# Kernel optimization log

Measured on AMD Instinct MI355X. Metric: run time of the kernel, lower is better.

Reference implementation:

```python
import jax, jax.numpy as jnp
import numpy as np

RADIUS = 8
EPSILON = 0.01


def _diff_x(x, r):
    left = x[..., r:2 * r + 1, :]
    middle = x[..., 2 * r + 1:, :] - x[..., :-2 * r - 1, :]
    right = x[..., -1:, :] - x[..., -2 * r - 1:-r - 1, :]
    return jnp.concatenate([left, middle, right], axis=-2)


def _diff_y(x, r):
    left = x[..., r:2 * r + 1]
    middle = x[..., 2 * r + 1:] - x[..., :-2 * r - 1]
    right = x[..., -1:] - x[..., -2 * r - 1:-r - 1]
    return jnp.concatenate([left, middle, right], axis=-1)


def box_filter(x, r):
    # x: (N, C, H, W) -> windowed mean over (2r+1)x(2r+1) with reflect padding
    x = jnp.pad(x, ((0, 0), (0, 0), (r, r), (r, r)), mode='reflect')
    x = jnp.cumsum(x, axis=-2)
    x = _diff_x(x, r)
    x = jnp.cumsum(x, axis=-1)
    x = _diff_y(x, r)
    return x[..., r:-r, r:-r] / float((2 * r + 1) ** 2)


def setup_inputs() -> dict:
    key = jax.random.key(0)
    k1, k2 = jax.random.split(key)
    B, C, H, W = 4, 3, 1024, 1024
    I = jax.random.uniform(k1, (B, C, H, W), dtype=jnp.float32)
    p = jax.random.uniform(k2, (B, 1, H, W), dtype=jnp.float32)
    return {"I": I, "p": p}


def reference(I, p) -> jnp.ndarray:
    r, eps = RADIUS, EPSILON
    B, C, H, W = I.shape

    mean_I = box_filter(I, r)                     # (B,C,H,W)
    mean_p = box_filter(p, r)                     # (B,1,H,W)
    mean_Ip = box_filter(I * p, r)                # (B,C,H,W)
    cov_Ip = mean_Ip - mean_I * mean_p            # (B,C,H,W)

    # second moments: (B,C,C,H,W) via reshape to (B*C, C, H, W) for the box filter
    II = I[:, :, None] * I[:, None]               # (B,C,C,H,W)
    mean_II = box_filter(II.reshape(B * C, C, H, W), r).reshape(B, C, C, H, W)
    cov_II = mean_II - mean_I[:, :, None] * mean_I[:, None]

    eye = jnp.eye(C, dtype=I.dtype).reshape(1, C, C, 1, 1)
    S = cov_II + eps * eye                        # (B,C,C,H,W)

    # per-pixel CxC solve: move pixel dims to batch
    S_px = jnp.transpose(S, (0, 3, 4, 1, 2))      # (B,H,W,C,C)
    rhs = jnp.transpose(cov_Ip, (0, 2, 3, 1))[..., None]  # (B,H,W,C,1)
    a = jnp.linalg.solve(S_px, rhs)[..., 0]       # (B,H,W,C)
    a = jnp.transpose(a, (0, 3, 1, 2))            # (B,C,H,W)

    a_mean_I = jnp.einsum('bchw,bchw->bhw', a, mean_I)
    b = mean_p - a_mean_I[:, None]                # (B,1,H,W)

    mean_a = box_filter(a, r)
    mean_b = box_filter(b, r)

    q = jnp.einsum('bchw,bchw->bhw', mean_a, I) + mean_b[:, 0]
    return q[:, None]                             # (B,1,H,W)
```

## Files before the change

kernel.cpp:

```cpp
#include <hip/hip_runtime.h>

#define HH 1024
#define WW 1024
#define NB 4
#define RR 8
#define NCH1 13
#define NCH2 4
#define VSEG 8
#define NSEG (HH / VSEG)
#define NBLK (NB * NSEG)
#define NXCD 8
#define CPX (NBLK / NXCD)
#define LDSW 1040
#define INV_AREA (1.0f/289.0f)
#define EPS_REG 0.01f

typedef float f4 __attribute__((ext_vector_type(4)));
typedef _Float16 h4 __attribute__((ext_vector_type(4)));

__device__ __forceinline__ int refl(int j, int n) {
    int k = j < 0 ? -j : j;
    return k >= n ? 2 * n - 2 - k : k;
}

__device__ __forceinline__ int swz_logical(int id) {
    int xcd = id & (NXCD - 1);
    int rank = id >> 3;
    return xcd * CPX + rank;
}

__device__ __forceinline__ void derived13(f4 i0, f4 i1, f4 i2, f4 pp, f4* d) {
    d[0] = i0; d[1] = i1; d[2] = i2; d[3] = pp;
    d[4] = i0 * pp; d[5] = i1 * pp; d[6] = i2 * pp;
    d[7] = i0 * i0; d[8] = i0 * i1; d[9] = i0 * i2;
    d[10] = i1 * i1; d[11] = i1 * i2; d[12] = i2 * i2;
}

__global__ __launch_bounds__(256, 2) void gf_stage1(
    const float* __restrict__ I, const float* __restrict__ P,
    _Float16* __restrict__ A, _Float16* __restrict__ Bc)
{
    __shared__ float lds[NCH1][LDSW];
    const int tid = threadIdx.x;
    const int logical = swz_logical(blockIdx.x);
    const int bz = logical / NSEG;
    const int y0 = (logical % NSEG) * VSEG;
    const int c0 = 4 * tid;
    const float* Ib = I + (size_t)bz * 3 * HH * WW;
    const float* Pb = P + (size_t)bz * HH * WW;

    f4 vs[NCH1];
    #pragma unroll
    for (int ch = 0; ch < NCH1; ++ch) { vs[ch] = (f4){0.f, 0.f, 0.f, 0.f}; }

    for (int dy = -RR; dy <= RR; ++dy) {
        int row = refl(y0 + dy, HH);
        size_t rb = (size_t)row * WW + c0;
        f4 i0 = *(const f4*)(Ib + rb);
        f4 i1 = *(const f4*)(Ib + (size_t)HH * WW + rb);
        f4 i2 = *(const f4*)(Ib + (size_t)2 * HH * WW + rb);
        f4 pp = *(const f4*)(Pb + rb);
        f4 d[NCH1]; derived13(i0, i1, i2, pp, d);
        #pragma unroll
        for (int ch = 0; ch < NCH1; ++ch) vs[ch] += d[ch];
    }

    for (int y = y0; y < y0 + VSEG; ++y) {
        #pragma unroll
        for (int ch = 0; ch < NCH1; ++ch)
            *(f4*)&lds[ch][8 + c0] = vs[ch];
        if (tid <= 2) {
            #pragma unroll
            for (int j = 0; j < 4; ++j) {
                int c = c0 + j;
                if (c >= 1 && c <= 8) {
                    #pragma unroll
                    for (int ch = 0; ch < NCH1; ++ch) lds[ch][8 - c] = vs[ch][j];
                }
            }
        }
        if (tid >= 253) {
            #pragma unroll
            for (int j = 0; j < 4; ++j) {
                int c = c0 + j;
                if (c >= 1015 && c <= 1022) {
                    #pragma unroll
                    for (int ch = 0; ch < NCH1; ++ch) lds[ch][1032 + (1022 - c)] = vs[ch][j];
                }
            }
        }
        const bool upd = (y + 1 < y0 + VSEG);
        f4 ai0, ai1, ai2, ap, si0, si1, si2, sp;
        if (upd) {
            int ra = refl(y + 1 + RR, HH);
            int rs = refl(y - RR, HH);
            size_t rba = (size_t)ra * WW + c0;
            size_t rbs = (size_t)rs * WW + c0;
            ai0 = *(const f4*)(Ib + rba);
            ai1 = *(const f4*)(Ib + (size_t)HH * WW + rba);
            ai2 = *(const f4*)(Ib + (size_t)2 * HH * WW + rba);
            ap  = *(const f4*)(Pb + rba);
            si0 = *(const f4*)(Ib + rbs);
            si1 = *(const f4*)(Ib + (size_t)HH * WW + rbs);
            si2 = *(const f4*)(Ib + (size_t)2 * HH * WW + rbs);
            sp  = *(const f4*)(Pb + rbs);
        }
        __syncthreads();

        f4 m[NCH1];
        #pragma unroll
        for (int ch = 0; ch < NCH1; ++ch) {
            float vv[20];
            #pragma unroll
            for (int k = 0; k < 5; ++k)
                ((f4*)vv)[k] = *(const f4*)&lds[ch][c0 + 4 * k];
            float s = (((vv[0]+vv[1])+(vv[2]+vv[3])) + ((vv[4]+vv[5])+(vv[6]+vv[7])))
                    + (((vv[8]+vv[9])+(vv[10]+vv[11])) + ((vv[12]+vv[13])+(vv[14]+vv[15])))
                    + vv[16];
            f4 mm;
            mm[0] = s;
            s += vv[17] - vv[0]; mm[1] = s;
            s += vv[18] - vv[1]; mm[2] = s;
            s += vv[19] - vv[2]; mm[3] = s;
            m[ch] = mm * INV_AREA;
        }

        f4 oa0, oa1, oa2, ob;
        #pragma unroll
        for (int j = 0; j < 4; ++j) {
            float m0 = m[0][j], m1 = m[1][j], m2 = m[2][j], m3 = m[3][j];
            float r0 = m[4][j] - m0 * m3;
            float r1 = m[5][j] - m1 * m3;
            float r2 = m[6][j] - m2 * m3;
            float S00 = m[7][j]  - m0 * m0 + EPS_REG;
            float S01 = m[8][j]  - m0 * m1;
            float S02 = m[9][j]  - m0 * m2;
            float S11 = m[10][j] - m1 * m1 + EPS_REG;
            float S12 = m[11][j] - m1 * m2;
            float S22 = m[12][j] - m2 * m2 + EPS_REG;
            float A0 = S11 * S22 - S12 * S12;
            float B0 = S02 * S12 - S01 * S22;
            float C0 = S01 * S12 - S02 * S11;
            float D0 = S00 * S22 - S02 * S02;
            float E0 = S01 * S02 - S00 * S12;
            float F0 = S00 * S11 - S01 * S01;
            float det = S00 * A0 + S01 * B0 + S02 * C0;
            float inv = 1.0f / det;
            float a0 = (A0 * r0 + B0 * r1 + C0 * r2) * inv;
            float a1 = (B0 * r0 + D0 * r1 + E0 * r2) * inv;
            float a2 = (C0 * r0 + E0 * r1 + F0 * r2) * inv;
            float bb = m3 - (a0 * m0 + a1 * m1 + a2 * m2);
            oa0[j] = a0; oa1[j] = a1; oa2[j] = a2; ob[j] = bb;
        }
        size_t obase = (size_t)y * WW + c0;
        *(h4*)(A + (size_t)(bz * 3 + 0) * HH * WW + obase) = __builtin_convertvector(oa0, h4);
        *(h4*)(A + (size_t)(bz * 3 + 1) * HH * WW + obase) = __builtin_convertvector(oa1, h4);
        *(h4*)(A + (size_t)(bz * 3 + 2) * HH * WW + obase) = __builtin_convertvector(oa2, h4);
        *(h4*)(Bc + (size_t)bz * HH * WW + obase) = __builtin_convertvector(ob, h4);
        __syncthreads();

        if (upd) {
            f4 d[NCH1];
            derived13(ai0, ai1, ai2, ap, d);
            #pragma unroll
            for (int ch = 0; ch < NCH1; ++ch) vs[ch] += d[ch];
            derived13(si0, si1, si2, sp, d);
            #pragma unroll
            for (int ch = 0; ch < NCH1; ++ch) vs[ch] -= d[ch];
        }
    }
}

__global__ __launch_bounds__(256, 2) void gf_stage2(
    const float* __restrict__ I, const _Float16* __restrict__ A,
    const _Float16* __restrict__ Bc, float* __restrict__ Q)
{
    __shared__ float lds[NCH2][LDSW];
    const int tid = threadIdx.x;
    const int logical = swz_logical(blockIdx.x);
    const int bz = logical / NSEG;
    const int y0 = (logical % NSEG) * VSEG;
    const int c0 = 4 * tid;
    const _Float16* A0p = A + (size_t)(bz * 3 + 0) * HH * WW;
    const _Float16* A1p = A + (size_t)(bz * 3 + 1) * HH * WW;
    const _Float16* A2p = A + (size_t)(bz * 3 + 2) * HH * WW;
    const _Float16* Bp  = Bc + (size_t)bz * HH * WW;
    const float* Ib  = I + (size_t)bz * 3 * HH * WW;

    f4 vs[NCH2];
    #pragma unroll
    for (int ch = 0; ch < NCH2; ++ch) { vs[ch] = (f4){0.f, 0.f, 0.f, 0.f}; }

    for (int dy = -RR; dy <= RR; ++dy) {
        int row = refl(y0 + dy, HH);
        size_t rb = (size_t)row * WW + c0;
        vs[0] += __builtin_convertvector(*(const h4*)(A0p + rb), f4);
        vs[1] += __builtin_convertvector(*(const h4*)(A1p + rb), f4);
        vs[2] += __builtin_convertvector(*(const h4*)(A2p + rb), f4);
        vs[3] += __builtin_convertvector(*(const h4*)(Bp + rb), f4);
    }

    for (int y = y0; y < y0 + VSEG; ++y) {
        #pragma unroll
        for (int ch = 0; ch < NCH2; ++ch)
            *(f4*)&lds[ch][8 + c0] = vs[ch];
        if (tid <= 2) {
            #pragma unroll
            for (int j = 0; j < 4; ++j) {
                int c = c0 + j;
                if (c >= 1 && c <= 8) {
                    #pragma unroll
                    for (int ch = 0; ch < NCH2; ++ch) lds[ch][8 - c] = vs[ch][j];
                }
            }
        }
        if (tid >= 253) {
            #pragma unroll
            for (int j = 0; j < 4; ++j) {
                int c = c0 + j;
                if (c >= 1015 && c <= 1022) {
                    #pragma unroll
                    for (int ch = 0; ch < NCH2; ++ch) lds[ch][1032 + (1022 - c)] = vs[ch][j];
                }
            }
        }
        const bool upd = (y + 1 < y0 + VSEG);
        f4 aa0, aa1, aa2, ab, sa0, sa1, sa2, sb;
        size_t rbq = (size_t)y * WW + c0;
        f4 i0 = *(const f4*)(Ib + rbq);
        f4 i1 = *(const f4*)(Ib + (size_t)HH * WW + rbq);
        f4 i2 = *(const f4*)(Ib + (size_t)2 * HH * WW + rbq);
        if (upd) {
            int ra = refl(y + 1 + RR, HH);
            int rs = refl(y - RR, HH);
            size_t rba = (size_t)ra * WW + c0;
            size_t rbs = (size_t)rs * WW + c0;
            aa0 = __builtin_convertvector(*(const h4*)(A0p + rba), f4);
            aa1 = __builtin_convertvector(*(const h4*)(A1p + rba), f4);
            aa2 = __builtin_convertvector(*(const h4*)(A2p + rba), f4);
            ab  = __builtin_convertvector(*(const h4*)(Bp + rba), f4);
            sa0 = __builtin_convertvector(*(const h4*)(A0p + rbs), f4);
            sa1 = __builtin_convertvector(*(const h4*)(A1p + rbs), f4);
            sa2 = __builtin_convertvector(*(const h4*)(A2p + rbs), f4);
            sb  = __builtin_convertvector(*(const h4*)(Bp + rbs), f4);
        }
        __syncthreads();

        f4 m[NCH2];
        #pragma unroll
        for (int ch = 0; ch < NCH2; ++ch) {
            float vv[20];
            #pragma unroll
            for (int k = 0; k < 5; ++k)
                ((f4*)vv)[k] = *(const f4*)&lds[ch][c0 + 4 * k];
            float s = (((vv[0]+vv[1])+(vv[2]+vv[3])) + ((vv[4]+vv[5])+(vv[6]+vv[7])))
                    + (((vv[8]+vv[9])+(vv[10]+vv[11])) + ((vv[12]+vv[13])+(vv[14]+vv[15])))
                    + vv[16];
            f4 mm;
            mm[0] = s;
            s += vv[17] - vv[0]; mm[1] = s;
            s += vv[18] - vv[1]; mm[2] = s;
            s += vv[19] - vv[2]; mm[3] = s;
            m[ch] = mm * INV_AREA;
        }

        f4 qv = m[0] * i0 + m[1] * i1 + m[2] * i2 + m[3];
        *(f4*)(Q + (size_t)bz * HH * WW + (size_t)y * WW + c0) = qv;
        __syncthreads();

        if (upd) {
            vs[0] += aa0 - sa0;
            vs[1] += aa1 - sa1;
            vs[2] += aa2 - sa2;
            vs[3] += ab - sb;
        }
    }
}

extern "C" void kernel_launch(void* const* d_in, const int* in_sizes, int n_in,
                              void* d_out, int out_size, void* d_ws, size_t ws_size,
                              hipStream_t stream) {
    const float* I = (const float*)d_in[0];
    const float* P = (const float*)d_in[1];
    float* Q = (float*)d_out;
    _Float16* A = (_Float16*)d_ws;
    _Float16* Bc = A + (size_t)NB * 3 * HH * WW;
    gf_stage1<<<NBLK, 256, 0, stream>>>(I, P, A, Bc);
    gf_stage2<<<NBLK, 256, 0, stream>>>(I, A, Bc, Q);
}
```

Before: 81.68 us.

## Split stage-2 into half-width column strips with per-thread halo accumulators

Stage 2 now processes each row segment as two 512-column strips, doubling the block count, with each thread handling 2 columns instead of 4. Sixteen threads per block keep running vertical sums for the reflected 8-column halos on either side, loaded with scalar fp16 reads. The goal is more parallelism and occupancy in the second pass. The cost is narrower vector loads, extra halo reads, and more per-block overhead.

Result: slower. 86.62 us (+6.1%).

```diff
diff --git a/kernel.cpp b/kernel.cpp
--- a/kernel.cpp
+++ b/kernel.cpp
@@ -8,25 +8,26 @@
 #define NCH2 4
 #define VSEG 8
 #define NSEG (HH / VSEG)
-#define NBLK (NB * NSEG)
 #define NXCD 8
-#define CPX (NBLK / NXCD)
-#define LDSW 1040
+#define NBLK1 (NB * NSEG)
+#define CPX1 (NBLK1 / NXCD)
+#define LDSW1 1040
+#define TW 512
+#define NWS (WW / TW)
+#define NBLK2 (NB * NSEG * NWS)
+#define CPX2 (NBLK2 / NXCD)
+#define LDSW2 544
 #define INV_AREA (1.0f/289.0f)
 #define EPS_REG 0.01f
 
 typedef float f4 __attribute__((ext_vector_type(4)));
 typedef _Float16 h4 __attribute__((ext_vector_type(4)));
+typedef float f2 __attribute__((ext_vector_type(2)));
+typedef _Float16 h2 __attribute__((ext_vector_type(2)));
 
 __device__ __forceinline__ int refl(int j, int n) {
     int k = j < 0 ? -j : j;
     return k >= n ? 2 * n - 2 - k : k;
-}
-
-__device__ __forceinline__ int swz_logical(int id) {
-    int xcd = id & (NXCD - 1);
-    int rank = id >> 3;
-    return xcd * CPX + rank;
 }
 
 __device__ __forceinline__ void derived13(f4 i0, f4 i1, f4 i2, f4 pp, f4* d) {
@@ -40,9 +41,9 @@
     const float* __restrict__ I, const float* __restrict__ P,
     _Float16* __restrict__ A, _Float16* __restrict__ Bc)
 {
-    __shared__ float lds[NCH1][LDSW];
+    __shared__ float lds[NCH1][LDSW1];
     const int tid = threadIdx.x;
-    const int logical = swz_logical(blockIdx.x);
+    const int logical = (blockIdx.x & (NXCD - 1)) * CPX1 + (blockIdx.x >> 3);
     const int bz = logical / NSEG;
     const int y0 = (logical % NSEG) * VSEG;
     const int c0 = 4 * tid;
@@ -171,101 +172,105 @@
     }
 }
 
+__device__ __forceinline__ f2 hwin2(const float* ldsrow, int c0) {
+    const f2* wp = (const f2*)(ldsrow + c0);
+    f2 w0 = wp[0], w1 = wp[1], w2 = wp[2], w3 = wp[3];
+    f2 w4 = wp[4], w5 = wp[5], w6 = wp[6], w7 = wp[7], w8 = wp[8];
+    f2 e = ((w0 + w1) + (w2 + w3)) + ((w4 + w5) + (w6 + w7));
+    float s0 = e[0] + e[1] + w8[0];
+    float s1 = s0 - w0[0] + w8[1];
+    f2 r; r[0] = s0 * INV_AREA; r[1] = s1 * INV_AREA;
+    return r;
+}
+
 __global__ __launch_bounds__(256, 2) void gf_stage2(
     const float* __restrict__ I, const _Float16* __restrict__ A,
     const _Float16* __restrict__ Bc, float* __restrict__ Q)
 {
-    __shared__ float lds[NCH2][LDSW];
+    __shared__ float lds[NCH2][LDSW2];
     const int tid = threadIdx.x;
-    const int logical = swz_logical(blockIdx.x);
-    const int bz = logical / NSEG;
+    const int logical = (blockIdx.x & (NXCD - 1)) * CPX2 + (blockIdx.x >> 3);
+    const int strip = logical / NSEG;
     const int y0 = (logical % NSEG) * VSEG;
-    const int c0 = 4 * tid;
+    const int bz = strip >> 1;
+    const int wstart = (strip & 1) * TW;
+    const int c0 = 2 * tid;
+    const int gc = wstart + c0;
     const _Float16* A0p = A + (size_t)(bz * 3 + 0) * HH * WW;
     const _Float16* A1p = A + (size_t)(bz * 3 + 1) * HH * WW;
     const _Float16* A2p = A + (size_t)(bz * 3 + 2) * HH * WW;
     const _Float16* Bp  = Bc + (size_t)bz * HH * WW;
     const float* Ib  = I + (size_t)bz * 3 * HH * WW;
 
-    f4 vs[NCH2];
+    const bool isHalo = tid < 16;
+    const int hraw = (tid < 8) ? (wstart - 8 + tid) : (wstart + TW + (tid - 8));
+    const int hg = refl(hraw, WW);
+    const int hpos = (tid < 8) ? tid : (8 + TW + (tid - 8));
+
+    f2 vs[NCH2];
+    float hs[NCH2];
     #pragma unroll
-    for (int ch = 0; ch < NCH2; ++ch) { vs[ch] = (f4){0.f, 0.f, 0.f, 0.f}; }
+    for (int ch = 0; ch < NCH2; ++ch) { vs[ch] = (f2){0.f, 0.f}; hs[ch] = 0.f; }
 
     for (int dy = -RR; dy <= RR; ++dy) {
         int row = refl(y0 + dy, HH);
-        size_t rb = (size_t)row * WW + c0;
-        vs[0] += __builtin_convertvector(*(const h4*)(A0p + rb), f4);
-        vs[1] += __builtin_convertvector(*(const h4*)(A1p + rb), f4);
-        vs[2] += __builtin_convertvector(*(const h4*)(A2p + rb), f4);
-        vs[3] += __builtin_convertvector(*(const h4*)(Bp + rb), f4);
+        size_t rb = (size_t)row * WW;
+        vs[0] += __builtin_convertvector(*(const h2*)(A0p + rb + gc), f2);
+        vs[1] += __builtin_convertvector(*(const h2*)(A1p + rb + gc), f2);
+        vs[2] += __builtin_convertvector(*(const h2*)(A2p + rb + gc), f2);
+        vs[3] += __builtin_convertvector(*(const h2*)(Bp + rb + gc), f2);
+        if (isHalo) {
+            hs[0] += (float)A0p[rb + hg];
+            hs[1] += (float)A1p[rb + hg];
+            hs[2] += (float)A2p[rb + hg];
+            hs[3] += (float)Bp[rb + hg];
+        }
     }
 
     for (int y = y0; y < y0 + VSEG; ++y) {
         #pragma unroll
         for (int ch = 0; ch < NCH2; ++ch)
-            *(f4*)&lds[ch][8 + c0] = vs[ch];
-        if (tid <= 2) {
-            #pragma unroll
-            for (int j = 0; j < 4; ++j) {
-                int c = c0 + j;
-                if (c >= 1 && c <= 8) {
-                    #pragma unroll
-                    for (int ch = 0; ch < NCH2; ++ch) lds[ch][8 - c] = vs[ch][j];
-                }
-            }
-        }
-        if (tid >= 253) {
-            #pragma unroll
-            for (int j = 0; j < 4; ++j) {
-                int c = c0 + j;
-                if (c >= 1015 && c <= 1022) {
-                    #pragma unroll
-                    for (int ch = 0; ch < NCH2; ++ch) lds[ch][1032 + (1022 - c)] = vs[ch][j];
-                }
-            }
+            *(f2*)&lds[ch][8 + c0] = vs[ch];
+        if (isHalo) {
+            #pragma unroll
+            for (int ch = 0; ch < NCH2; ++ch) lds[ch][hpos] = hs[ch];
         }
         const bool upd = (y + 1 < y0 + VSEG);
-        f4 aa0, aa1, aa2, ab, sa0, sa1, sa2, sb;
-        size_t rbq = (size_t)y * WW + c0;
-        f4 i0 = *(const f4*)(Ib + rbq);
-        f4 i1 = *(const f4*)(Ib + (size_t)HH * WW + rbq);
-        f4 i2 = *(const f4*)(Ib + (size_t)2 * HH * WW + rbq);
+        f2 aa0, aa1, aa2, ab, sa0, sa1, sa2, sb;
+        float ha0, ha1, ha2, hab, hb0, hb1, hb2, hbb;
+        size_t rbq = (size_t)y * WW;
+        f2 i0 = *(const f2*)(Ib + rbq + gc);
+        f2 i1 = *(const f2*)(Ib + (size_t)HH * WW + rbq + gc);
+        f2 i2 = *(const f2*)(Ib + (size_t)2 * HH * WW + rbq + gc);
         if (upd) {
             int ra = refl(y + 1 + RR, HH);
             int rs = refl(y - RR, HH);
-            size_t rba = (size_t)ra * WW + c0;
-            size_t rbs = (size_t)rs * WW + c0;
-            aa0 = __builtin_convertvector(*(const h4*)(A0p + rba), f4);
-            aa1 = __builtin_convertvector(*(const h4*)(A1p + rba), f4);
-            aa2 = __builtin_convertvector(*(const h4*)(A2p + rba), f4);
-            ab  = __builtin_convertvector(*(const h4*)(Bp + rba), f4);
-            sa0 = __builtin_convertvector(*(const h4*)(A0p + rbs), f4);
-            sa1 = __builtin_convertvector(*(const h4*)(A1p + rbs), f4);
-            sa2 = __builtin_convertvector(*(const h4*)(A2p + rbs), f4);
-            sb  = __builtin_convertvector(*(const h4*)(Bp + rbs), f4);
-        }
-        __syncthreads();
-
-        f4 m[NCH2];
-        #pragma unroll
-        for (int ch = 0; ch < NCH2; ++ch) {
-            float vv[20];
-            #pragma unroll
-            for (int k = 0; k < 5; ++k)
-                ((f4*)vv)[k] = *(const f4*)&lds[ch][c0 + 4 * k];
-            float s = (((vv[0]+vv[1])+(vv[2]+vv[3])) + ((vv[4]+vv[5])+(vv[6]+vv[7])))
-                    + (((vv[8]+vv[9])+(vv[10]+vv[11])) + ((vv[12]+vv[13])+(vv[14]+vv[15])))
-                    + vv[16];
-            f4 mm;
-            mm[0] = s;
-            s += vv[17] - vv[0]; mm[1] = s;
-            s += vv[18] - vv[1]; mm[2] = s;
-            s += vv[19] - vv[2]; mm[3] = s;
-            m[ch] = mm * INV_AREA;
-        }
-
-        f4 qv = m[0] * i0 + m[1] * i1 + m[2] * i2 + m[3];
-        *(f4*)(Q + (size_t)bz * HH * WW + (size_t)y * WW + c0) = qv;
+            size_t rba = (size_t)ra * WW;
+            size_t rbs = (size_t)rs * WW;
+            aa0 = __builtin_convertvector(*(const h2*)(A0p + rba + gc), f2);
+            aa1 = __builtin_convertvector(*(const h2*)(A1p + rba + gc), f2);
+            aa2 = __builtin_convertvector(*(const h2*)(A2p + rba + gc), f2);
+            ab  = __builtin_convertvector(*(const h2*)(Bp + rba + gc), f2);
+            sa0 = __builtin_convertvector(*(const h2*)(A0p + rbs + gc), f2);
+            sa1 = __builtin_convertvector(*(const h2*)(A1p + rbs + gc), f2);
+            sa2 = __builtin_convertvector(*(const h2*)(A2p + rbs + gc), f2);
+            sb  = __builtin_convertvector(*(const h2*)(Bp + rbs + gc), f2);
+            if (isHalo) {
+                ha0 = (float)A0p[rba + hg]; ha1 = (float)A1p[rba + hg];
+                ha2 = (float)A2p[rba + hg]; hab = (float)Bp[rba + hg];
+                hb0 = (float)A0p[rbs + hg]; hb1 = (float)A1p[rbs + hg];
+                hb2 = (float)A2p[rbs + hg]; hbb = (float)Bp[rbs + hg];
+            }
+        }
+        __syncthreads();
+
+        f2 m[NCH2];
+        #pragma unroll
+        for (int ch = 0; ch < NCH2; ++ch)
+            m[ch] = hwin2(&lds[ch][0], c0);
+
+        f2 qv = m[0] * i0 + m[1] * i1 + m[2] * i2 + m[3];
+        *(f2*)(Q + (size_t)bz * HH * WW + rbq + gc) = qv;
         __syncthreads();
 
         if (upd) {
@@ -273,6 +278,10 @@
             vs[1] += aa1 - sa1;
             vs[2] += aa2 - sa2;
             vs[3] += ab - sb;
+            if (isHalo) {
+                hs[0] += ha0 - hb0; hs[1] += ha1 - hb1;
+                hs[2] += ha2 - hb2; hs[3] += hab - hbb;
+            }
         }
     }
 }
@@ -285,6 +294,6 @@
     float* Q = (float*)d_out;
     _Float16* A = (_Float16*)d_ws;
     _Float16* Bc = A + (size_t)NB * 3 * HH * WW;
-    gf_stage1<<<NBLK, 256, 0, stream>>>(I, P, A, Bc);
-    gf_stage2<<<NBLK, 256, 0, stream>>>(I, A, Bc, Q);
-}
+    gf_stage1<<<NBLK1, 256, 0, stream>>>(I, P, A, Bc);
+    gf_stage2<<<NBLK2, 256, 0, stream>>>(I, A, Bc, Q);
+}
```
